# Optimization experiments

Measured on AMD Instinct MI355X. Metric: run time of the kernel, lower is better.

Reference implementation:

```python
import jax, jax.numpy as jnp
import numpy as np

H = 40  # HIDDEN_SIZE


def _gru_layer(x_tbi, Wih, Whh, bih, bhh):
    """PyTorch-convention GRU layer. x_tbi: (T, B, I). Returns (ys (T,B,H), h_T (B,H)).
    Gate order in stacked weights is (r, z, n) as in torch.nn.GRU:
      r = sigmoid(W_ir x + b_ir + W_hr h + b_hr)
      z = sigmoid(W_iz x + b_iz + W_hz h + b_hz)
      n = tanh(W_in x + b_in + r * (W_hn h + b_hn))
      h' = (1 - z) * n + z * h
    """
    # Precompute all input projections in one big GEMM: (T,B,3H)
    xg = jnp.einsum('tbi,gi->tbg', x_tbi, Wih) + bih
    B = x_tbi.shape[1]
    h0 = jnp.zeros((B, H), x_tbi.dtype)

    def step(h, xg_t):
        hg = h @ Whh.T + bhh                       # (B, 3H)
        xr, xz, xn = jnp.split(xg_t, 3, axis=-1)
        hr, hz, hn = jnp.split(hg, 3, axis=-1)
        r = jax.nn.sigmoid(xr + hr)
        z = jax.nn.sigmoid(xz + hz)
        n = jnp.tanh(xn + r * hn)
        h_new = (1.0 - z) * n + z * h
        return h_new, h_new

    hT, ys = jax.lax.scan(step, h0, xg)
    return ys, hT


def setup_inputs() -> dict:
    key = jax.random.key(0)
    ks = jax.random.split(key, 9)
    B, T, I = 4096, 256, 16
    s = 1.0 / np.sqrt(H)  # torch GRU init: U(-1/sqrt(H), 1/sqrt(H))
    u = lambda k, shape: jax.random.uniform(k, shape, jnp.float32, -s, s)
    return {
        "x": jax.random.normal(ks[0], (B, T, I), jnp.float32),
        "Wih0": u(ks[1], (3 * H, I)),
        "Whh0": u(ks[2], (3 * H, H)),
        "bih0": u(ks[3], (3 * H,)),
        "bhh0": u(ks[4], (3 * H,)),
        "Wih1": u(ks[5], (3 * H, H)),
        "Whh1": u(ks[6], (3 * H, H)),
        "bih1": u(ks[7], (3 * H,)),
        "bhh1": u(ks[8], (3 * H,)),
    }


def reference(x, Wih0, Whh0, bih0, bhh0, Wih1, Whh1, bih1, bhh1):
    # batch_first input (B,T,I) -> time-major (T,B,I) for scan
    x_tbi = jnp.transpose(x, (1, 0, 2))
    y0, _ = _gru_layer(x_tbi, Wih0, Whh0, bih0, bhh0)   # layer 0 full sequence
    _, hT = _gru_layer(y0, Wih1, Whh1, bih1, bhh1)      # layer 1 final state
    return hT  # (B, H) == h[-1]
```

## Files before the change

kernel.cpp:

```cpp
#include <hip/hip_runtime.h>

#define T_STEPS 256
#define HID 40
#define EPB 16
#define NTHR 1024
#define R0 72
#define R1 104
#define P0 (16 * R0)
#define P1 (16 * R1)
#define OL1 (2 * P0)
#define STOT (2 * P0 + 2 * P1)

typedef __attribute__((ext_vector_type(8))) short bf16x8;
typedef __attribute__((ext_vector_type(4))) float f32x4;

__device__ __forceinline__ unsigned short bf16_rne(float v) {
    unsigned int x = __float_as_uint(v);
    unsigned int r = x + 0x7FFFu + ((x >> 16) & 1u);
    return (unsigned short)(r >> 16);
}
__device__ __forceinline__ unsigned short bf16_cvt(float v) {
    unsigned int r;
    asm("v_cvt_pk_bf16_f32 %0, %1, %2" : "=v"(r) : "v"(v), "v"(v));
    return (unsigned short)r;
}
__device__ __forceinline__ float sigm(float v) {
    return __builtin_amdgcn_rcpf(1.0f + __builtin_amdgcn_exp2f(-1.4426950408889634f * v));
}
__device__ __forceinline__ float tanh_f(float v) {
    return 1.0f - 2.0f * __builtin_amdgcn_rcpf(__builtin_amdgcn_exp2f(2.8853900817779268f * v) + 1.0f);
}

#define MF(A_, B_, C_) C_ = __builtin_amdgcn_mfma_f32_16x16x32_bf16(A_, B_, C_, 0, 0, 0)
#define PINV(v) asm volatile("" : "+v"(v))

__device__ bf16x8 afrag(const float* Whh, const float* Wih, int KX,
                        int rh, int rx, int c, int qrow) {
    bf16x8 f;
    #pragma unroll
    for (int j = 0; j < 8; ++j) f[j] = 0;
    #pragma unroll
    for (int j = 0; j < 8; ++j) {
        const int k = 32 * c + qrow * 8 + j;
        if (k < 40) {
            if (rh >= 0) f[j] = (short)bf16_rne(Whh[rh * 40 + k]);
        } else if (k < 40 + KX) {
            if (rx >= 0) f[j] = (short)bf16_rne(Wih[rx * KX + (k - 40)]);
        }
    }
    return f;
}

__global__ __launch_bounds__(NTHR, 4)
void gru2_kernel(const float* __restrict__ x,
                 const float* __restrict__ Wih0, const float* __restrict__ Whh0,
                 const float* __restrict__ bih0, const float* __restrict__ bhh0,
                 const float* __restrict__ Wih1, const float* __restrict__ Whh1,
                 const float* __restrict__ bih1, const float* __restrict__ bhh1,
                 float* __restrict__ out)
{
    __shared__ __align__(16) unsigned short S[STOT];

    const int tid  = threadIdx.x;
    const int wid  = tid >> 6;
    const int l    = tid & 63;
    const int col  = l & 15;
    const int qrow = l >> 4;
    const int pm   = l & 15;
    const int ps   = pm & 3;
    const int pu   = pm >> 2;
    const int e0   = blockIdx.x * EPB;

    const bool isL1 = wid >= 6;
    const int  NT   = (!isL1 && wid < 4) ? 2 : 1;
    const int  TA   = isL1 ? (wid - 6) : (wid < 4 ? 2 * wid : wid + 4);
    const int  TB   = (NT == 2) ? TA + 1 : TA;
    const bool dB   = (NT != 2);

    const float* Whh = isL1 ? Whh1 : Whh0;
    const float* Wih = isL1 ? Wih1 : Wih0;
    const float* bih = isL1 ? bih1 : bih0;
    const float* bhh = isL1 ? bhh1 : bhh0;
    const int KX = isL1 ? 40 : 16;

    const int uA = 4 * TA + pu;
    const int rhA = (ps == 2) ? -1 : (ps == 0 ? uA : ps == 1 ? 40 + uA : 80 + uA);
    const int rxA = (ps == 3) ? -1 : (ps == 0 ? uA : ps == 1 ? 40 + uA : 80 + uA);
    const int uB = 4 * TB + pu;
    const int rhB = (dB || ps == 2) ? -1 : (ps == 0 ? uB : ps == 1 ? 40 + uB : 80 + uB);
    const int rxB = (dB || ps == 3) ? -1 : (ps == 0 ? uB : ps == 1 ? 40 + uB : 80 + uB);

    bf16x8 F0, F1, F2, F3;
    if (!isL1) {
        F0 = afrag(Whh, Wih, KX, rhA, rxA, 0, qrow);
        F1 = afrag(Whh, Wih, KX, rhA, rxA, 1, qrow);
        F2 = afrag(Whh, Wih, KX, rhB, rxB, 0, qrow);
        F3 = afrag(Whh, Wih, KX, rhB, rxB, 1, qrow);
    } else {
        F0 = afrag(Whh, Wih, KX, rhA, rxA, 0, qrow);
        F1 = afrag(Whh, Wih, KX, rhA, rxA, 1, qrow);
        F2 = afrag(Whh, Wih, KX, rhA, rxA, 2, qrow);
        F3 = afrag(Whh, Wih, KX, -1, -1, 0, qrow);
    }
    const int ucA = 4 * TA + qrow;
    const int ucB = 4 * TB + qrow;
    f32x4 BBA, BBB;
    BBA[0] = bih[ucA] + bhh[ucA];
    BBA[1] = bih[40 + ucA] + bhh[40 + ucA];
    BBA[2] = bih[80 + ucA];
    BBA[3] = bhh[80 + ucA];
    BBB[0] = dB ? 0.f : (bih[ucB] + bhh[ucB]);
    BBB[1] = dB ? 0.f : (bih[40 + ucB] + bhh[40 + ucB]);
    BBB[2] = dB ? 0.f : bih[80 + ucB];
    BBB[3] = dB ? 0.f : bhh[80 + ucB];

    PINV(F0); PINV(F1); PINV(F2); PINV(F3);
    PINV(BBA); PINV(BBB);

    const int rdl = isL1 ? (OL1 + col * R1 + qrow * 8) : (col * R0 + qrow * 8);
    const int w0b = col * R0;
    const int w1b = OL1 + col * R1;
    unsigned short* Sb = &S[0];
    float hA_ = 0.f, hB_ = 0.f;

#define GATE_L0(C, U, H, WP_) { \
    const float r_ = sigm(C[0]); \
    const float z_ = sigm(C[1]); \
    const float n_ = tanh_f(C[2] + r_ * C[3]); \
    H = n_ + z_ * (H - n_); \
    const unsigned short hb_ = bf16_cvt(H); \
    Sb[w0b + (WP_) * P0 + (U)] = hb_; \
    Sb[w1b + (WP_) * P1 + 40 + (U)] = hb_; }
#define GATE_L1(C, U, H, WP_) { \
    const float r_ = sigm(C[0]); \
    const float z_ = sigm(C[1]); \
    const float n_ = tanh_f(C[2] + r_ * C[3]); \
    H = n_ + z_ * (H - n_); \
    Sb[w1b + (WP_) * P1 + (U)] = bf16_cvt(H); }

    for (int idx = tid; idx < STOT; idx += NTHR) Sb[idx] = 0;
    __syncthreads();
    const bool xth = tid < 256;
    const int xe = tid >> 4, xk = tid & 15;
    const float* xrow = x + (size_t)(e0 + xe) * (T_STEPS * 16) + xk;
    float xold = 0.f;
    if (xth) {
        Sb[xe * R0 + 40 + xk] = bf16_cvt(xrow[0]);
        xold = xrow[16];
    }
    __syncthreads();

#define BODY(RP) { \
    float xnew = 0.f; \
    if (xth && t + 2 < T_STEPS) xnew = xrow[(t + 2) * 16]; \
    if (!isL1) { \
        const bf16x8 S0 = *(const bf16x8*)(Sb + rdl + (RP) * P0); \
        const bf16x8 S1 = *(const bf16x8*)(Sb + rdl + (RP) * P0 + 32); \
        if (t < T_STEPS) { \
            f32x4 c = __builtin_amdgcn_mfma_f32_16x16x32_bf16(F0, S0, BBA, 0, 0, 0); \
            MF(F1, S1, c); \
            GATE_L0(c, ucA, hA_, (1 - (RP))); \
            if (NT == 2) { \
                f32x4 d = __builtin_amdgcn_mfma_f32_16x16x32_bf16(F2, S0, BBB, 0, 0, 0); \
                MF(F3, S1, d); \
                GATE_L0(d, ucB, hB_, (1 - (RP))); \
            } \
        } \
    } else { \
        const bf16x8 S0 = *(const bf16x8*)(Sb + rdl + (RP) * P1); \
        const bf16x8 S1 = *(const bf16x8*)(Sb + rdl + (RP) * P1 + 32); \
        const bf16x8 S2 = *(const bf16x8*)(Sb + rdl + (RP) * P1 + 64); \
        f32x4 c = __builtin_amdgcn_mfma_f32_16x16x32_bf16(F0, S0, BBA, 0, 0, 0); \
        MF(F1, S1, c); MF(F2, S2, c); \
        if (t > 0) GATE_L1(c, ucA, hA_, (1 - (RP))); \
    } \
    if (xth && t < T_STEPS - 1) { \
        Sb[xe * R0 + (1 - (RP)) * P0 + 40 + xk] = bf16_cvt(xold); \
    } \
    xold = xnew; \
    ++t; \
    __syncthreads(); }

    int t = 0;
    #pragma unroll 1
    for (int it = 0; it < 128; ++it) {
        BODY(0)
        BODY(1)
    }
    BODY(0)

    if (isL1) {
        out[(size_t)(e0 + col) * HID + ucA] = hA_;
    }
}

extern "C" void kernel_launch(void* const* d_in, const int* in_sizes, int n_in,
                              void* d_out, int out_size, void* d_ws, size_t ws_size,
                              hipStream_t stream) {
    const float* x    = (const float*)d_in[0];
    const float* Wih0 = (const float*)d_in[1];
    const float* Whh0 = (const float*)d_in[2];
    const float* bih0 = (const float*)d_in[3];
    const float* bhh0 = (const float*)d_in[4];
    const float* Wih1 = (const float*)d_in[5];
    const float* Whh1 = (const float*)d_in[6];
    const float* bih1 = (const float*)d_in[7];
    const float* bhh1 = (const float*)d_in[8];
    float* out = (float*)d_out;

    dim3 grid(4096 / EPB), block(NTHR);
    hipLaunchKernelGGL(gru2_kernel, grid, block, 0, stream,
                       x, Wih0, Whh0, bih0, bhh0, Wih1, Whh1, bih1, bhh1, out);
}
```

Baseline: 223.2 us.

## Halve block to 8 waves, give each wave 2-3 gate tiles, inject x via registers

Reduces the block from 16 to 8 waves, with 4 waves per layer each handling two or three 4-unit gate tiles, so the per-step barrier synchronizes fewer waves. The input x is prefetched four steps ahead into registers and packed straight into the B operand fragment instead of being staged through LDS by a separate thread group. The LDS layout is unified into a single row stride, and layer 1 reads layer-0 hidden state from the shared buffers. The cost is more serial MFMA and gate work per wave on the recurrent critical path, plus higher register pressure, which the launch bounds acknowledge by targeting fewer blocks per CU.

```diff
diff --git a/kernel.cpp b/kernel.cpp
--- a/kernel.cpp
+++ b/kernel.cpp
@@ -3,16 +3,16 @@
 #define T_STEPS 256
 #define HID 40
 #define EPB 16
-#define NTHR 1024
-#define R0 72
-#define R1 104
-#define P0 (16 * R0)
-#define P1 (16 * R1)
-#define OL1 (2 * P0)
-#define STOT (2 * P0 + 2 * P1)
+#define NTHR 512
+#define RR 56
+#define PP (16 * RR)
+#define OL1 (2 * PP)
+#define STOT (4 * PP)
 
 typedef __attribute__((ext_vector_type(8))) short bf16x8;
 typedef __attribute__((ext_vector_type(4))) float f32x4;
+typedef __attribute__((ext_vector_type(8))) float f32x8;
+typedef __attribute__((ext_vector_type(4))) unsigned int u32x4;
 
 __device__ __forceinline__ unsigned short bf16_rne(float v) {
     unsigned int x = __float_as_uint(v);
@@ -51,7 +51,7 @@
     return f;
 }
 
-__global__ __launch_bounds__(NTHR, 4)
+__global__ __launch_bounds__(NTHR, 2)
 void gru2_kernel(const float* __restrict__ x,
                  const float* __restrict__ Wih0, const float* __restrict__ Whh0,
                  const float* __restrict__ bih0, const float* __restrict__ bhh0,
@@ -66,16 +66,14 @@
     const int l    = tid & 63;
     const int col  = l & 15;
     const int qrow = l >> 4;
-    const int pm   = l & 15;
-    const int ps   = pm & 3;
-    const int pu   = pm >> 2;
+    const int ps   = (l & 15) & 3;
+    const int pu   = (l & 15) >> 2;
     const int e0   = blockIdx.x * EPB;
 
-    const bool isL1 = wid >= 6;
-    const int  NT   = (!isL1 && wid < 4) ? 2 : 1;
-    const int  TA   = isL1 ? (wid - 6) : (wid < 4 ? 2 * wid : wid + 4);
-    const int  TB   = (NT == 2) ? TA + 1 : TA;
-    const bool dB   = (NT != 2);
+    const bool isL1 = wid >= 4;
+    const int  m    = isL1 ? wid - 4 : wid;
+    const int  NTIL = (m < 2) ? 3 : 2;
+    const int  Tb   = (m < 2) ? 3 * m : 6 + 2 * (m - 2);
 
     const float* Whh = isL1 ? Whh1 : Whh0;
     const float* Wih = isL1 ? Wih1 : Wih0;
@@ -83,114 +81,166 @@
     const float* bhh = isL1 ? bhh1 : bhh0;
     const int KX = isL1 ? 40 : 16;
 
-    const int uA = 4 * TA + pu;
-    const int rhA = (ps == 2) ? -1 : (ps == 0 ? uA : ps == 1 ? 40 + uA : 80 + uA);
-    const int rxA = (ps == 3) ? -1 : (ps == 0 ? uA : ps == 1 ? 40 + uA : 80 + uA);
-    const int uB = 4 * TB + pu;
-    const int rhB = (dB || ps == 2) ? -1 : (ps == 0 ? uB : ps == 1 ? 40 + uB : 80 + uB);
-    const int rxB = (dB || ps == 3) ? -1 : (ps == 0 ? uB : ps == 1 ? 40 + uB : 80 + uB);
-
-    bf16x8 F0, F1, F2, F3;
+    bf16x8 ZF;
+    #pragma unroll
+    for (int j = 0; j < 8; ++j) ZF[j] = 0;
+    bf16x8 F00=ZF,F01=ZF,F02=ZF, F10=ZF,F11=ZF,F12=ZF, F20=ZF,F21=ZF,F22=ZF;
+    f32x4 BB0, BB1, BB2;
+    {
+#define RRX(u, RH, RX) \
+        const int RH = (ps == 2) ? -1 : (ps == 0 ? (u) : ps == 1 ? 40 + (u) : 80 + (u)); \
+        const int RX = (ps == 3) ? -1 : (ps == 0 ? (u) : ps == 1 ? 40 + (u) : 80 + (u));
+        {
+            const int u0 = 4 * (Tb + 0) + pu;
+            RRX(u0, rh0, rx0);
+            F00 = afrag(Whh, Wih, KX, rh0, rx0, 0, qrow);
+            F01 = afrag(Whh, Wih, KX, rh0, rx0, 1, qrow);
+            if (isL1) F02 = afrag(Whh, Wih, KX, rh0, rx0, 2, qrow);
+        }
+        {
+            const int u1 = 4 * (Tb + 1) + pu;
+            RRX(u1, rh1, rx1);
+            F10 = afrag(Whh, Wih, KX, rh1, rx1, 0, qrow);
+            F11 = afrag(Whh, Wih, KX, rh1, rx1, 1, qrow);
+            if (isL1) F12 = afrag(Whh, Wih, KX, rh1, rx1, 2, qrow);
+        }
+        if (NTIL == 3) {
+            const int u2 = 4 * (Tb + 2) + pu;
+            RRX(u2, rh2, rx2);
+            F20 = afrag(Whh, Wih, KX, rh2, rx2, 0, qrow);
+            F21 = afrag(Whh, Wih, KX, rh2, rx2, 1, qrow);
+            if (isL1) F22 = afrag(Whh, Wih, KX, rh2, rx2, 2, qrow);
+        }
+        const int uc0 = 4 * (Tb + 0) + qrow;
+        const int uc1 = 4 * (Tb + 1) + qrow;
+        BB0[0] = bih[uc0] + bhh[uc0];
+        BB0[1] = bih[40 + uc0] + bhh[40 + uc0];
+        BB0[2] = bih[80 + uc0];
+        BB0[3] = bhh[80 + uc0];
+        BB1[0] = bih[uc1] + bhh[uc1];
+        BB1[1] = bih[40 + uc1] + bhh[40 + uc1];
+        BB1[2] = bih[80 + uc1];
+        BB1[3] = bhh[80 + uc1];
+        if (NTIL == 3) {
+            const int uc2 = 4 * (Tb + 2) + qrow;
+            BB2[0] = bih[uc2] + bhh[uc2];
+            BB2[1] = bih[40 + uc2] + bhh[40 + uc2];
+            BB2[2] = bih[80 + uc2];
+            BB2[3] = bhh[80 + uc2];
+        } else {
+            BB2[0] = BB2[1] = BB2[2] = BB2[3] = 0.f;
+        }
+    }
+    PINV(F00); PINV(F01); PINV(F02);
+    PINV(F10); PINV(F11); PINV(F12);
+    PINV(F20); PINV(F21); PINV(F22);
+    PINV(BB0); PINV(BB1); PINV(BB2);
+
+    int r0p0, r0p1, r1p0, r1p1, r2p0, r2p1;
     if (!isL1) {
-        F0 = afrag(Whh, Wih, KX, rhA, rxA, 0, qrow);
-        F1 = afrag(Whh, Wih, KX, rhA, rxA, 1, qrow);
-        F2 = afrag(Whh, Wih, KX, rhB, rxB, 0, qrow);
-        F3 = afrag(Whh, Wih, KX, rhB, rxB, 1, qrow);
+        r0p0 = col * RR + 8 * qrow;  r0p1 = r0p0 + PP;
+        r1p0 = col * RR + 32;        r1p1 = r1p0 + PP;
+        r2p0 = 0;                    r2p1 = 0;
     } else {
-        F0 = afrag(Whh, Wih, KX, rhA, rxA, 0, qrow);
-        F1 = afrag(Whh, Wih, KX, rhA, rxA, 1, qrow);
-        F2 = afrag(Whh, Wih, KX, rhA, rxA, 2, qrow);
-        F3 = afrag(Whh, Wih, KX, -1, -1, 0, qrow);
-    }
-    const int ucA = 4 * TA + qrow;
-    const int ucB = 4 * TB + qrow;
-    f32x4 BBA, BBB;
-    BBA[0] = bih[ucA] + bhh[ucA];
-    BBA[1] = bih[40 + ucA] + bhh[40 + ucA];
-    BBA[2] = bih[80 + ucA];
-    BBA[3] = bhh[80 + ucA];
-    BBB[0] = dB ? 0.f : (bih[ucB] + bhh[ucB]);
-    BBB[1] = dB ? 0.f : (bih[40 + ucB] + bhh[40 + ucB]);
-    BBB[2] = dB ? 0.f : bih[80 + ucB];
-    BBB[3] = dB ? 0.f : bhh[80 + ucB];
-
-    PINV(F0); PINV(F1); PINV(F2); PINV(F3);
-    PINV(BBA); PINV(BBB);
-
-    const int rdl = isL1 ? (OL1 + col * R1 + qrow * 8) : (col * R0 + qrow * 8);
-    const int w0b = col * R0;
-    const int w1b = OL1 + col * R1;
+        auto ga = [&](int g, int p) -> int {
+            if (g < 5)  return OL1 + p * PP + col * RR + 8 * g;
+            if (g < 10) return p * PP + col * RR + 8 * (g - 5);
+            return p * PP + col * RR;
+        };
+        r0p0 = ga(qrow, 0);     r0p1 = ga(qrow, 1);
+        r1p0 = ga(4 + qrow, 0); r1p1 = ga(4 + qrow, 1);
+        r2p0 = ga(8 + qrow, 0); r2p1 = ga(8 + qrow, 1);
+    }
+    const int wof = (isL1 ? OL1 : 0) + col * RR + 4 * Tb + qrow;
+    const bool usex = (qrow == 1) || (qrow == 2);
     unsigned short* Sb = &S[0];
-    float hA_ = 0.f, hB_ = 0.f;
-
-#define GATE_L0(C, U, H, WP_) { \
+    float hA0 = 0.f, hA1 = 0.f, hA2 = 0.f;
+
+    for (int idx = tid; idx < STOT; idx += NTHR) Sb[idx] = 0;
+
+    const float* xrow = x + (size_t)(e0 + col) * (T_STEPS * 16) + ((qrow == 2) ? 8 : 0);
+    f32x8 XA, XB, XC, XD;
+    #pragma unroll
+    for (int j = 0; j < 8; ++j) { XA[j] = 0.f; XB[j] = 0.f; XC[j] = 0.f; XD[j] = 0.f; }
+    if (!isL1) {
+        XA = *(const f32x8*)(xrow);
+        XB = *(const f32x8*)(xrow + 16);
+        XC = *(const f32x8*)(xrow + 32);
+        XD = *(const f32x8*)(xrow + 48);
+    }
+    __syncthreads();
+
+#define GMATH(C, H) \
     const float r_ = sigm(C[0]); \
     const float z_ = sigm(C[1]); \
     const float n_ = tanh_f(C[2] + r_ * C[3]); \
-    H = n_ + z_ * (H - n_); \
-    const unsigned short hb_ = bf16_cvt(H); \
-    Sb[w0b + (WP_) * P0 + (U)] = hb_; \
-    Sb[w1b + (WP_) * P1 + 40 + (U)] = hb_; }
-#define GATE_L1(C, U, H, WP_) { \
-    const float r_ = sigm(C[0]); \
-    const float z_ = sigm(C[1]); \
-    const float n_ = tanh_f(C[2] + r_ * C[3]); \
-    H = n_ + z_ * (H - n_); \
-    Sb[w1b + (WP_) * P1 + (U)] = bf16_cvt(H); }
-
-    for (int idx = tid; idx < STOT; idx += NTHR) Sb[idx] = 0;
-    __syncthreads();
-    const bool xth = tid < 256;
-    const int xe = tid >> 4, xk = tid & 15;
-    const float* xrow = x + (size_t)(e0 + xe) * (T_STEPS * 16) + xk;
-    float xold = 0.f;
-    if (xth) {
-        Sb[xe * R0 + 40 + xk] = bf16_cvt(xrow[0]);
-        xold = xrow[16];
-    }
-    __syncthreads();
-
-#define BODY(RP) { \
-    float xnew = 0.f; \
-    if (xth && t + 2 < T_STEPS) xnew = xrow[(t + 2) * 16]; \
+    H = n_ + z_ * (H - n_);
+
+#define BODY(RP, XQ) { \
     if (!isL1) { \
-        const bf16x8 S0 = *(const bf16x8*)(Sb + rdl + (RP) * P0); \
-        const bf16x8 S1 = *(const bf16x8*)(Sb + rdl + (RP) * P0 + 32); \
+        const bf16x8 S0 = *(const bf16x8*)(Sb + r0p##RP); \
+        bf16x8 S1 = *(const bf16x8*)(Sb + r1p##RP); \
         if (t < T_STEPS) { \
-            f32x4 c = __builtin_amdgcn_mfma_f32_16x16x32_bf16(F0, S0, BBA, 0, 0, 0); \
-            MF(F1, S1, c); \
-            GATE_L0(c, ucA, hA_, (1 - (RP))); \
-            if (NT == 2) { \
-                f32x4 d = __builtin_amdgcn_mfma_f32_16x16x32_bf16(F2, S0, BBB, 0, 0, 0); \
-                MF(F3, S1, d); \
-                GATE_L0(d, ucB, hB_, (1 - (RP))); \
+            unsigned int xw0, xw1, xw2, xw3; \
+            asm("v_cvt_pk_bf16_f32 %0, %1, %2" : "=v"(xw0) : "v"(XQ[0]), "v"(XQ[1])); \
+            asm("v_cvt_pk_bf16_f32 %0, %1, %2" : "=v"(xw1) : "v"(XQ[2]), "v"(XQ[3])); \
+            asm("v_cvt_pk_bf16_f32 %0, %1, %2" : "=v"(xw2) : "v"(XQ[4]), "v"(XQ[5])); \
+            asm("v_cvt_pk_bf16_f32 %0, %1, %2" : "=v"(xw3) : "v"(XQ[6]), "v"(XQ[7])); \
+            if (t + 4 < T_STEPS) XQ = *(const f32x8*)(xrow + (t + 4) * 16); \
+            u32x4 s1u = *(const u32x4*)&S1; \
+            s1u[0] = usex ? xw0 : s1u[0]; \
+            s1u[1] = usex ? xw1 : s1u[1]; \
+            s1u[2] = usex ? xw2 : s1u[2]; \
+            s1u[3] = usex ? xw3 : s1u[3]; \
+            S1 = *(const bf16x8*)&s1u; \
+            f32x4 c0 = __builtin_amdgcn_mfma_f32_16x16x32_bf16(F00, S0, BB0, 0, 0, 0); \
+            MF(F01, S1, c0); \
+            f32x4 c1 = __builtin_amdgcn_mfma_f32_16x16x32_bf16(F10, S0, BB1, 0, 0, 0); \
+            MF(F11, S1, c1); \
+            { GMATH(c0, hA0); Sb[(1 - (RP)) * PP + wof + 0] = bf16_cvt(hA0); } \
+            { GMATH(c1, hA1); Sb[(1 - (RP)) * PP + wof + 4] = bf16_cvt(hA1); } \
+            if (NTIL == 3) { \
+                f32x4 c2 = __builtin_amdgcn_mfma_f32_16x16x32_bf16(F20, S0, BB2, 0, 0, 0); \
+                MF(F21, S1, c2); \
+                GMATH(c2, hA2); Sb[(1 - (RP)) * PP + wof + 8] = bf16_cvt(hA2); \
             } \
         } \
     } else { \
-        const bf16x8 S0 = *(const bf16x8*)(Sb + rdl + (RP) * P1); \
-        const bf16x8 S1 = *(const bf16x8*)(Sb + rdl + (RP) * P1 + 32); \
-        const bf16x8 S2 = *(const bf16x8*)(Sb + rdl + (RP) * P1 + 64); \
-        f32x4 c = __builtin_amdgcn_mfma_f32_16x16x32_bf16(F0, S0, BBA, 0, 0, 0); \
-        MF(F1, S1, c); MF(F2, S2, c); \
-        if (t > 0) GATE_L1(c, ucA, hA_, (1 - (RP))); \
+        const bf16x8 S0 = *(const bf16x8*)(Sb + r0p##RP); \
+        const bf16x8 S1 = *(const bf16x8*)(Sb + r1p##RP); \
+        const bf16x8 S2 = *(const bf16x8*)(Sb + r2p##RP); \
+        f32x4 c0 = __builtin_amdgcn_mfma_f32_16x16x32_bf16(F00, S0, BB0, 0, 0, 0); \
+        MF(F01, S1, c0); MF(F02, S2, c0); \
+        f32x4 c1 = __builtin_amdgcn_mfma_f32_16x16x32_bf16(F10, S0, BB1, 0, 0, 0); \
+        MF(F11, S1, c1); MF(F12, S2, c1); \
+        if (t > 0) { \
+            { GMATH(c0, hA0); Sb[(1 - (RP)) * PP + wof + 0] = bf16_cvt(hA0); } \
+            { GMATH(c1, hA1); Sb[(1 - (RP)) * PP + wof + 4] = bf16_cvt(hA1); } \
+        } \
+        if (NTIL == 3) { \
+            f32x4 c2 = __builtin_amdgcn_mfma_f32_16x16x32_bf16(F20, S0, BB2, 0, 0, 0); \
+            MF(F21, S1, c2); MF(F22, S2, c2); \
+            if (t > 0) { GMATH(c2, hA2); Sb[(1 - (RP)) * PP + wof + 8] = bf16_cvt(hA2); } \
+        } \
     } \
-    if (xth && t < T_STEPS - 1) { \
-        Sb[xe * R0 + (1 - (RP)) * P0 + 40 + xk] = bf16_cvt(xold); \
-    } \
-    xold = xnew; \
     ++t; \
     __syncthreads(); }
 
     int t = 0;
     #pragma unroll 1
-    for (int it = 0; it < 128; ++it) {
-        BODY(0)
-        BODY(1)
-    }
-    BODY(0)
+    for (int it = 0; it < 64; ++it) {
+        BODY(0, XA)
+        BODY(1, XB)
+        BODY(0, XC)
+        BODY(1, XD)
+    }
+    BODY(0, XA)
 
     if (isL1) {
-        out[(size_t)(e0 + col) * HID + ucA] = hA_;
+        float* op = out + (size_t)(e0 + col) * HID + 4 * Tb + qrow;
+        op[0] = hA0;
+        op[4] = hA1;
+        if (NTIL == 3) op[8] = hA2;
     }
 }
 
```

Result: slower. 233.7 us (+4.7%).

## Collapse GRU block to one wave per layer with batched-step ring buffer

Applied to the files above, without the earlier changes.

Each 16-sequence block now runs with two waves, one per layer. Each wave handles all ten hidden-unit tiles, with their weight fragments held in registers. Hidden states go into a 16-slot LDS ring buffer, so layer 1 trails layer 0 by four steps and only one block barrier is needed per four timesteps instead of one per step. Input rows are prefetched as 8-float vectors and packed straight into the MFMA operand. This trades cross-wave parallelism and SIMD occupancy for far fewer barriers and more independent MFMA chains inside each wave, and it raises register pressure.

```diff
diff --git a/kernel.cpp b/kernel.cpp
--- a/kernel.cpp
+++ b/kernel.cpp
@@ -3,16 +3,17 @@
 #define T_STEPS 256
 #define HID 40
 #define EPB 16
-#define NTHR 1024
-#define R0 72
-#define R1 104
-#define P0 (16 * R0)
-#define P1 (16 * R1)
-#define OL1 (2 * P0)
-#define STOT (2 * P0 + 2 * P1)
+#define NTHR 128
+#define RRH 56
+#define SLOT (16 * RRH)
+#define NSLOT 16
+#define H1B (NSLOT * SLOT)
+#define STOT (H1B + SLOT)
 
 typedef __attribute__((ext_vector_type(8))) short bf16x8;
 typedef __attribute__((ext_vector_type(4))) float f32x4;
+typedef __attribute__((ext_vector_type(8))) float f32x8;
+typedef __attribute__((ext_vector_type(4))) unsigned int u32x4;
 
 __device__ __forceinline__ unsigned short bf16_rne(float v) {
     unsigned int x = __float_as_uint(v);
@@ -51,7 +52,7 @@
     return f;
 }
 
-__global__ __launch_bounds__(NTHR, 4)
+__global__ __launch_bounds__(NTHR, 1)
 void gru2_kernel(const float* __restrict__ x,
                  const float* __restrict__ Wih0, const float* __restrict__ Whh0,
                  const float* __restrict__ bih0, const float* __restrict__ bhh0,
@@ -66,16 +67,10 @@
     const int l    = tid & 63;
     const int col  = l & 15;
     const int qrow = l >> 4;
-    const int pm   = l & 15;
-    const int ps   = pm & 3;
-    const int pu   = pm >> 2;
+    const int ps   = col & 3;
+    const int pu   = col >> 2;
     const int e0   = blockIdx.x * EPB;
-
-    const bool isL1 = wid >= 6;
-    const int  NT   = (!isL1 && wid < 4) ? 2 : 1;
-    const int  TA   = isL1 ? (wid - 6) : (wid < 4 ? 2 * wid : wid + 4);
-    const int  TB   = (NT == 2) ? TA + 1 : TA;
-    const bool dB   = (NT != 2);
+    const bool isL1 = (wid == 1);
 
     const float* Whh = isL1 ? Whh1 : Whh0;
     const float* Wih = isL1 ? Wih1 : Wih0;
@@ -83,114 +78,128 @@
     const float* bhh = isL1 ? bhh1 : bhh0;
     const int KX = isL1 ? 40 : 16;
 
-    const int uA = 4 * TA + pu;
-    const int rhA = (ps == 2) ? -1 : (ps == 0 ? uA : ps == 1 ? 40 + uA : 80 + uA);
-    const int rxA = (ps == 3) ? -1 : (ps == 0 ? uA : ps == 1 ? 40 + uA : 80 + uA);
-    const int uB = 4 * TB + pu;
-    const int rhB = (dB || ps == 2) ? -1 : (ps == 0 ? uB : ps == 1 ? 40 + uB : 80 + uB);
-    const int rxB = (dB || ps == 3) ? -1 : (ps == 0 ? uB : ps == 1 ? 40 + uB : 80 + uB);
-
-    bf16x8 F0, F1, F2, F3;
+    bf16x8 F[10][3];
+    f32x4  BB[10];
+    float  H[10];
+    #pragma unroll
+    for (int m = 0; m < 10; ++m) {
+        const int u  = 4 * m + pu;
+        const int rh = (ps == 2) ? -1 : (ps == 0 ? u : ps == 1 ? 40 + u : 80 + u);
+        const int rx = (ps == 3) ? -1 : (ps == 0 ? u : ps == 1 ? 40 + u : 80 + u);
+        F[m][0] = afrag(Whh, Wih, KX, rh, rx, 0, qrow);
+        F[m][1] = afrag(Whh, Wih, KX, rh, rx, 1, qrow);
+        F[m][2] = afrag(Whh, Wih, KX, rh, rx, 2, qrow);
+        const int uc = 4 * m + qrow;
+        BB[m][0] = bih[uc] + bhh[uc];
+        BB[m][1] = bih[40 + uc] + bhh[40 + uc];
+        BB[m][2] = bih[80 + uc];
+        BB[m][3] = bhh[80 + uc];
+        H[m] = 0.f;
+    }
+    #pragma unroll
+    for (int m = 0; m < 10; ++m) {
+        PINV(F[m][0]); PINV(F[m][1]); PINV(F[m][2]); PINV(BB[m]);
+    }
+
+    const int rdl0 = col * RRH + 8 * qrow;
+    const int rdl1 = col * RRH + 32;
+    const int w0l  = col * RRH + qrow;
+    const int rdh1 = H1B + col * RRH + 8 * qrow;
+    const int off1 = (qrow == 0) ? (H1B + col * RRH + 32) : (col * RRH + 8 * (qrow - 1));
+    const int msk1 = (qrow == 0) ? 0 : -1;
+    const int off2 = (qrow == 0) ? (col * RRH + 24)
+                   : (qrow == 1) ? (col * RRH + 32) : (col * RRH);
+    const int w1l  = H1B + col * RRH + qrow;
+    const bool usex = (qrow == 1) || (qrow == 2);
+    unsigned short* Sb = &S[0];
+
+    for (int i = tid; i < STOT; i += NTHR) Sb[i] = 0;
+
+    const float* xrow = x + (size_t)(e0 + col) * (T_STEPS * 16) + ((qrow == 2) ? 8 : 0);
+    f32x8 XRa, XRb;
+    #pragma unroll
+    for (int j = 0; j < 8; ++j) { XRa[j] = 0.f; XRb[j] = 0.f; }
     if (!isL1) {
-        F0 = afrag(Whh, Wih, KX, rhA, rxA, 0, qrow);
-        F1 = afrag(Whh, Wih, KX, rhA, rxA, 1, qrow);
-        F2 = afrag(Whh, Wih, KX, rhB, rxB, 0, qrow);
-        F3 = afrag(Whh, Wih, KX, rhB, rxB, 1, qrow);
-    } else {
-        F0 = afrag(Whh, Wih, KX, rhA, rxA, 0, qrow);
-        F1 = afrag(Whh, Wih, KX, rhA, rxA, 1, qrow);
-        F2 = afrag(Whh, Wih, KX, rhA, rxA, 2, qrow);
-        F3 = afrag(Whh, Wih, KX, -1, -1, 0, qrow);
-    }
-    const int ucA = 4 * TA + qrow;
-    const int ucB = 4 * TB + qrow;
-    f32x4 BBA, BBB;
-    BBA[0] = bih[ucA] + bhh[ucA];
-    BBA[1] = bih[40 + ucA] + bhh[40 + ucA];
-    BBA[2] = bih[80 + ucA];
-    BBA[3] = bhh[80 + ucA];
-    BBB[0] = dB ? 0.f : (bih[ucB] + bhh[ucB]);
-    BBB[1] = dB ? 0.f : (bih[40 + ucB] + bhh[40 + ucB]);
-    BBB[2] = dB ? 0.f : bih[80 + ucB];
-    BBB[3] = dB ? 0.f : bhh[80 + ucB];
-
-    PINV(F0); PINV(F1); PINV(F2); PINV(F3);
-    PINV(BBA); PINV(BBB);
-
-    const int rdl = isL1 ? (OL1 + col * R1 + qrow * 8) : (col * R0 + qrow * 8);
-    const int w0b = col * R0;
-    const int w1b = OL1 + col * R1;
-    unsigned short* Sb = &S[0];
-    float hA_ = 0.f, hB_ = 0.f;
-
-#define GATE_L0(C, U, H, WP_) { \
+        XRa = *(const f32x8*)(xrow);
+        XRb = *(const f32x8*)(xrow + 16);
+    }
+    __syncthreads();
+
+#define GMATH(C, Hm) \
     const float r_ = sigm(C[0]); \
     const float z_ = sigm(C[1]); \
     const float n_ = tanh_f(C[2] + r_ * C[3]); \
-    H = n_ + z_ * (H - n_); \
-    const unsigned short hb_ = bf16_cvt(H); \
-    Sb[w0b + (WP_) * P0 + (U)] = hb_; \
-    Sb[w1b + (WP_) * P1 + 40 + (U)] = hb_; }
-#define GATE_L1(C, U, H, WP_) { \
-    const float r_ = sigm(C[0]); \
-    const float z_ = sigm(C[1]); \
-    const float n_ = tanh_f(C[2] + r_ * C[3]); \
-    H = n_ + z_ * (H - n_); \
-    Sb[w1b + (WP_) * P1 + (U)] = bf16_cvt(H); }
-
-    for (int idx = tid; idx < STOT; idx += NTHR) Sb[idx] = 0;
-    __syncthreads();
-    const bool xth = tid < 256;
-    const int xe = tid >> 4, xk = tid & 15;
-    const float* xrow = x + (size_t)(e0 + xe) * (T_STEPS * 16) + xk;
-    float xold = 0.f;
-    if (xth) {
-        Sb[xe * R0 + 40 + xk] = bf16_cvt(xrow[0]);
-        xold = xrow[16];
-    }
-    __syncthreads();
-
-#define BODY(RP) { \
-    float xnew = 0.f; \
-    if (xth && t + 2 < T_STEPS) xnew = xrow[(t + 2) * 16]; \
-    if (!isL1) { \
-        const bf16x8 S0 = *(const bf16x8*)(Sb + rdl + (RP) * P0); \
-        const bf16x8 S1 = *(const bf16x8*)(Sb + rdl + (RP) * P0 + 32); \
-        if (t < T_STEPS) { \
-            f32x4 c = __builtin_amdgcn_mfma_f32_16x16x32_bf16(F0, S0, BBA, 0, 0, 0); \
-            MF(F1, S1, c); \
-            GATE_L0(c, ucA, hA_, (1 - (RP))); \
-            if (NT == 2) { \
-                f32x4 d = __builtin_amdgcn_mfma_f32_16x16x32_bf16(F2, S0, BBB, 0, 0, 0); \
-                MF(F3, S1, d); \
-                GATE_L0(d, ucB, hB_, (1 - (RP))); \
-            } \
-        } \
-    } else { \
-        const bf16x8 S0 = *(const bf16x8*)(Sb + rdl + (RP) * P1); \
-        const bf16x8 S1 = *(const bf16x8*)(Sb + rdl + (RP) * P1 + 32); \
-        const bf16x8 S2 = *(const bf16x8*)(Sb + rdl + (RP) * P1 + 64); \
-        f32x4 c = __builtin_amdgcn_mfma_f32_16x16x32_bf16(F0, S0, BBA, 0, 0, 0); \
-        MF(F1, S1, c); MF(F2, S2, c); \
-        if (t > 0) GATE_L1(c, ucA, hA_, (1 - (RP))); \
+    Hm = n_ + z_ * (Hm - n_);
+
+#define L0STEP(J, XREG) { \
+    const int t   = 4 * b + (J); \
+    const int rsr = ((t - 1) & 15) * SLOT; \
+    const int wsr = (t & 15) * SLOT; \
+    const bf16x8 S0 = *(const bf16x8*)(Sb + rsr + rdl0); \
+    bf16x8 S1 = *(const bf16x8*)(Sb + rsr + rdl1); \
+    unsigned int xw0, xw1, xw2, xw3; \
+    asm("v_cvt_pk_bf16_f32 %0, %1, %2" : "=v"(xw0) : "v"(XREG[0]), "v"(XREG[1])); \
+    asm("v_cvt_pk_bf16_f32 %0, %1, %2" : "=v"(xw1) : "v"(XREG[2]), "v"(XREG[3])); \
+    asm("v_cvt_pk_bf16_f32 %0, %1, %2" : "=v"(xw2) : "v"(XREG[4]), "v"(XREG[5])); \
+    asm("v_cvt_pk_bf16_f32 %0, %1, %2" : "=v"(xw3) : "v"(XREG[6]), "v"(XREG[7])); \
+    if (t + 2 < T_STEPS) XREG = *(const f32x8*)(xrow + (t + 2) * 16); \
+    u32x4 s1u = *(const u32x4*)&S1; \
+    s1u[0] = usex ? xw0 : s1u[0]; \
+    s1u[1] = usex ? xw1 : s1u[1]; \
+    s1u[2] = usex ? xw2 : s1u[2]; \
+    s1u[3] = usex ? xw3 : s1u[3]; \
+    S1 = *(const bf16x8*)&s1u; \
+    _Pragma("unroll") \
+    for (int m = 0; m < 10; ++m) { \
+        f32x4 c = __builtin_amdgcn_mfma_f32_16x16x32_bf16(F[m][0], S0, BB[m], 0, 0, 0); \
+        MF(F[m][1], S1, c); \
+        GMATH(c, H[m]); \
+        Sb[wsr + w0l + 4 * m] = bf16_cvt(H[m]); \
     } \
-    if (xth && t < T_STEPS - 1) { \
-        Sb[xe * R0 + (1 - (RP)) * P0 + 40 + xk] = bf16_cvt(xold); \
+}
+
+#define L1STEP(J) { \
+    const int tt  = 4 * (b - 1) + (J); \
+    const int rsr = (tt & 15) * SLOT; \
+    const int a1  = off1 + (rsr & msk1); \
+    const int a2  = off2 + rsr; \
+    const bf16x8 S0 = *(const bf16x8*)(Sb + rdh1); \
+    const bf16x8 S1 = *(const bf16x8*)(Sb + a1); \
+    const bf16x8 S2 = *(const bf16x8*)(Sb + a2); \
+    _Pragma("unroll") \
+    for (int m = 0; m < 10; ++m) { \
+        f32x4 c = __builtin_amdgcn_mfma_f32_16x16x32_bf16(F[m][0], S0, BB[m], 0, 0, 0); \
+        MF(F[m][1], S1, c); \
+        MF(F[m][2], S2, c); \
+        GMATH(c, H[m]); \
+        Sb[w1l + 4 * m] = bf16_cvt(H[m]); \
     } \
-    xold = xnew; \
-    ++t; \
-    __syncthreads(); }
-
-    int t = 0;
+}
+
     #pragma unroll 1
-    for (int it = 0; it < 128; ++it) {
-        BODY(0)
-        BODY(1)
-    }
-    BODY(0)
+    for (int b = 0; b <= 64; ++b) {
+        if (!isL1) {
+            if (b < 64) {
+                L0STEP(0, XRa)
+                L0STEP(1, XRb)
+                L0STEP(2, XRa)
+                L0STEP(3, XRb)
+            }
+        } else {
+            if (b >= 1) {
+                L1STEP(0)
+                L1STEP(1)
+                L1STEP(2)
+                L1STEP(3)
+            }
+        }
+        __syncthreads();
+    }
 
     if (isL1) {
-        out[(size_t)(e0 + col) * HID + ucA] = hA_;
+        float* op = out + (size_t)(e0 + col) * HID + qrow;
+        #pragma unroll
+        for (int m = 0; m < 10; ++m) op[4 * m] = H[m];
     }
 }
 
```

After: 334.3 us. 49.8% more time.
